# Kernel tuning notes

Hardware: AMD Instinct MI355X
Metric: run time of the kernel (lower is better)

The kernel has to match this reference:

```python
import jax, jax.numpy as jnp
import numpy as np

N_NODES = 50000


def gcn_conv(x, edge_index, W, b):
    # PyG GCNConv: add self-loops, symmetric normalization, linear (no bias), scatter-add, + bias
    n = x.shape[0]
    loops = jnp.arange(n, dtype=edge_index.dtype)
    src = jnp.concatenate([edge_index[0], loops])
    dst = jnp.concatenate([edge_index[1], loops])
    deg = jax.ops.segment_sum(jnp.ones_like(dst, dtype=x.dtype), dst, num_segments=n)
    dinv = jnp.where(deg > 0, jax.lax.rsqrt(deg), 0.0)
    norm = dinv[src] * dinv[dst]                       # [E+N]
    h = x @ W                                          # [N, out]
    msg = h[src] * norm[:, None]                       # [E+N, out]
    return jax.ops.segment_sum(msg, dst, num_segments=n) + b


def setup_inputs() -> dict:
    key = jax.random.key(0)
    k1, k2, k3, k4, k5, k6 = jax.random.split(key, 6)
    z = jax.random.normal(k1, (N_NODES, 64), dtype=jnp.float32)
    edge_index = jax.random.randint(k2, (2, 1600000), 0, N_NODES, dtype=jnp.int64)
    # glorot-ish init for weights
    W1 = jax.random.normal(k3, (64, 128), dtype=jnp.float32) * (1.0 / np.sqrt(64))
    b1 = jnp.zeros((128,), dtype=jnp.float32)
    W2 = jax.random.normal(k4, (128, 64), dtype=jnp.float32) * (1.0 / np.sqrt(128))
    b2 = jnp.zeros((64,), dtype=jnp.float32)
    return {"z": z, "edge_index": edge_index, "W1": W1, "b1": b1, "W2": W2, "b2": b2}


def reference(z, edge_index, W1, b1, W2, b2):
    h = jax.nn.relu(gcn_conv(z, edge_index, W1, b1))
    x_hat = jax.nn.relu(gcn_conv(h, edge_index, W2, b2))
    return x_hat
```

## Files before the change

kernel.cpp:

```cpp
#include <hip/hip_runtime.h>
#include <hip/hip_fp16.h>


#define NBUK 196
#define NPAD (NBUK * 256)
#define BCAP 16384
#define SCAP 32
#define SSH 4
#define SCAP2 32
#define SENT 0xFFFFFFFFu
#define P1GRID 768

struct half4_t { __half2 lo, hi; };
struct half8_t { __half2 h0, h1, h2, h3; };

__global__ void zero_kernel(int* __restrict__ p, int n) {
    int i = blockIdx.x * blockDim.x + threadIdx.x;
    if (i < n) p[i] = 0;
}

__global__ __launch_bounds__(256) void pass1_kernel(
    const int* __restrict__ src, const int* __restrict__ dst,
    unsigned* __restrict__ bucketed, int* __restrict__ gcur,
    unsigned* __restrict__ ovf, int* __restrict__ novf, int E) {
    __shared__ unsigned stage[NBUK * SCAP];
    __shared__ int lcnt[NBUK];
    __shared__ int bbase[NBUK];
    __shared__ unsigned units[512];
    __shared__ int nunits;
    int tid = threadIdx.x;
    for (int i = tid; i < NBUK; i += 256) lcnt[i] = 0;
    if (tid == 0) nunits = 0;
    int per = (E + gridDim.x - 1) / gridDim.x;
    int lo = blockIdx.x * per, hi = min(E, lo + per);
    __syncthreads();
    for (int t0 = lo; t0 < hi; t0 += 2048) {
#pragma unroll
        for (int rep = 0; rep < 8; ++rep) {
            int i = t0 + rep * 256 + tid;
            if (i < hi) {
                int s = src[i], d = dst[i];
                int b = d >> 8;
                unsigned pk = (unsigned)(s & 0xFFFF) | ((unsigned)(d & 0xFF) << 16);
                int pos = atomicAdd(&lcnt[b], 1);
                if (pos < SCAP) {
                    stage[b * SCAP + pos] = pk;
                } else {
                    int op = atomicAdd(novf, 1);
                    if (op < 4096) ovf[op] = pk | ((unsigned)b << 24);
                    atomicSub(&lcnt[b], 1);
                }
            }
        }
        __syncthreads();
        if (tid < NBUK) {
            int c = min(lcnt[tid], SCAP);
            int f = c >> 4;
            if (f > 0) {
                bbase[tid] = atomicAdd(&gcur[tid], f * 16);
                int u0 = atomicAdd(&nunits, f);
                for (int g = 0; g < f; ++g) units[u0 + g] = ((unsigned)tid << 8) | g;
            }
        }
        __syncthreads();
        int nu = nunits;
        for (int u = tid >> 4; u < nu; u += 16) {
            unsigned ds = units[u];
            int b = ds >> 8, g = ds & 0xFF;
            int li = tid & 15;
            int idx = bbase[b] + g * 16 + li;
            if (idx < BCAP)
                bucketed[(size_t)b * BCAP + idx] = stage[b * SCAP + g * 16 + li];
        }
        __syncthreads();
        if (tid < NBUK) {
            int c = min(lcnt[tid], SCAP);
            int f = (c >> 4) << 4;
            int rem = c - f;
            for (int j = 0; j < rem; ++j) stage[tid * SCAP + j] = stage[tid * SCAP + f + j];
            lcnt[tid] = rem;
        }
        if (tid == 0) nunits = 0;
        __syncthreads();
    }
    if (tid < NBUK) {
        int c = min(lcnt[tid], SCAP);
        if (c > 0) {
            for (int j = c; j < 16; ++j) stage[tid * SCAP + j] = SENT;
            bbase[tid] = atomicAdd(&gcur[tid], 16);
            int u0 = atomicAdd(&nunits, 1);
            units[u0] = ((unsigned)tid << 8);
        }
    }
    __syncthreads();
    int nu = nunits;
    for (int u = tid >> 4; u < nu; u += 16) {
        unsigned ds = units[u];
        int b = ds >> 8, g = ds & 0xFF;
        int li = tid & 15;
        int idx = bbase[b] + g * 16 + li;
        if (idx < BCAP)
            bucketed[(size_t)b * BCAP + idx] = stage[b * SCAP + g * 16 + li];
    }
}

__global__ __launch_bounds__(256) void pass2_kernel(
    const unsigned* __restrict__ bucketed, const int* __restrict__ gcur,
    const unsigned* __restrict__ ovf, const int* __restrict__ novf,
    unsigned short* __restrict__ ellg, int* __restrict__ cnt4, int N) {
    __shared__ unsigned short ell[256 * SCAP2];
    __shared__ int lcnt[256];
    int b = blockIdx.x >> 2, q = blockIdx.x & 3;
    int tid = threadIdx.x;
    lcnt[tid] = 0;
    __syncthreads();
    int c = min(gcur[b], BCAP);
    int lo = (c * q) >> 2, hi = (c * (q + 1)) >> 2;
    const unsigned* bp = bucketed + (size_t)b * BCAP;
    for (int j = lo + tid; j < hi; j += 256) {
        unsigned e = bp[j];
        if (e == SENT) continue;
        int r = (e >> 16) & 0xFF;
        int p = atomicAdd(&lcnt[r], 1);
        if (p < SCAP2) ell[r * SCAP2 + p] = (unsigned short)(e & 0xFFFF);
    }
    if (q == 0) {
        int no = min(*novf, 4096);
        for (int j = tid; j < no; j += 256) {
            unsigned e = ovf[j];
            if ((int)(e >> 24) == b) {
                int r = (e >> 16) & 0xFF;
                int p = atomicAdd(&lcnt[r], 1);
                if (p < SCAP2) ell[r * SCAP2 + p] = (unsigned short)(e & 0xFFFF);
            }
        }
    }
    __syncthreads();
    int node = b * 256 + tid;
    if (node < N) cnt4[q * NPAD + node] = lcnt[tid];
    unsigned* eg = (unsigned*)(ellg + ((size_t)q * NPAD + b * 256) * SCAP2);
    const unsigned* el = (const unsigned*)ell;
    for (int k = tid; k < 256 * (SCAP2 / 2); k += 256) eg[k] = el[k];
}

__global__ void dinvps_kernel(const int* __restrict__ cnt4, const float* __restrict__ z,
                              float* __restrict__ dinv, half4_t* __restrict__ zp, int N) {
    int i = blockIdx.x * blockDim.x + threadIdx.x;
    if (i >= N * 16) return;
    int node = i >> 4;
    int deg = cnt4[node] + cnt4[NPAD + node] + cnt4[2 * NPAD + node] + cnt4[3 * NPAD + node];
    float w = rsqrtf((float)(deg + 1));
    if ((i & 15) == 0) dinv[node] = w;
    float4 v = reinterpret_cast<const float4*>(z)[i];
    half4_t h;
    h.lo = __floats2half2_rn(v.x * w, v.y * w);
    h.hi = __floats2half2_rn(v.z * w, v.w * w);
    zp[i] = h;
}

template <int EPI>
__global__ __launch_bounds__(256) void gatherv_kernel(
    const half8_t* __restrict__ rows, const int* __restrict__ cnt4,
    const unsigned short* __restrict__ ell, const float* __restrict__ dinv,
    const float* __restrict__ bias, void* __restrict__ outp, int N) {
    int node = (blockIdx.x * 256 + threadIdx.x) >> 6;
    int lane = threadIdx.x & 63;
    if (node >= N) return;
    int sg = lane >> 3, li = lane & 7;
    int stripe = sg >> 1, par = sg & 1;
    half8_t self = rows[node * 8 + li];
    float a0 = 0.f, a1 = 0.f, a2 = 0.f, a3 = 0.f, a4 = 0.f, a5 = 0.f, a6 = 0.f, a7 = 0.f;
    int cl = min(cnt4[stripe * NPAD + node], SCAP2);
    size_t base = ((size_t)stripe * NPAD + node) * SCAP2;
    int k = par;
    for (; k + 6 < cl; k += 8) {
        int s0 = ell[base + k];
        int s1 = ell[base + k + 2];
        int s2 = ell[base + k + 4];
        int s3 = ell[base + k + 6];
        half8_t v0 = rows[s0 * 8 + li];
        half8_t v1 = rows[s1 * 8 + li];
        half8_t v2 = rows[s2 * 8 + li];
        half8_t v3 = rows[s3 * 8 + li];
        float2 f;
        f = __half22float2(v0.h0); a0 += f.x; a1 += f.y;
        f = __half22float2(v0.h1); a2 += f.x; a3 += f.y;
        f = __half22float2(v0.h2); a4 += f.x; a5 += f.y;
        f = __half22float2(v0.h3); a6 += f.x; a7 += f.y;
        f = __half22float2(v1.h0); a0 += f.x; a1 += f.y;
        f = __half22float2(v1.h1); a2 += f.x; a3 += f.y;
        f = __half22float2(v1.h2); a4 += f.x; a5 += f.y;
        f = __half22float2(v1.h3); a6 += f.x; a7 += f.y;
        f = __half22float2(v2.h0); a0 += f.x; a1 += f.y;
        f = __half22float2(v2.h1); a2 += f.x; a3 += f.y;
        f = __half22float2(v2.h2); a4 += f.x; a5 += f.y;
        f = __half22float2(v2.h3); a6 += f.x; a7 += f.y;
        f = __half22float2(v3.h0); a0 += f.x; a1 += f.y;
        f = __half22float2(v3.h1); a2 += f.x; a3 += f.y;
        f = __half22float2(v3.h2); a4 += f.x; a5 += f.y;
        f = __half22float2(v3.h3); a6 += f.x; a7 += f.y;
    }
    if (k + 2 < cl) {
        int s0 = ell[base + k];
        int s1 = ell[base + k + 2];
        half8_t v0 = rows[s0 * 8 + li];
        half8_t v1 = rows[s1 * 8 + li];
        float2 f;
        f = __half22float2(v0.h0); a0 += f.x; a1 += f.y;
        f = __half22float2(v0.h1); a2 += f.x; a3 += f.y;
        f = __half22float2(v0.h2); a4 += f.x; a5 += f.y;
        f = __half22float2(v0.h3); a6 += f.x; a7 += f.y;
        f = __half22float2(v1.h0); a0 += f.x; a1 += f.y;
        f = __half22float2(v1.h1); a2 += f.x; a3 += f.y;
        f = __half22float2(v1.h2); a4 += f.x; a5 += f.y;
        f = __half22float2(v1.h3); a6 += f.x; a7 += f.y;
        k += 4;
    }
    if (k < cl) {
        int s = ell[base + k];
        half8_t v = rows[s * 8 + li];
        float2 f;
        f = __half22float2(v.h0); a0 += f.x; a1 += f.y;
        f = __half22float2(v.h1); a2 += f.x; a3 += f.y;
        f = __half22float2(v.h2); a4 += f.x; a5 += f.y;
        f = __half22float2(v.h3); a6 += f.x; a7 += f.y;
    }
#pragma unroll
    for (int off = 8; off < 64; off <<= 1) {
        a0 += __shfl_xor(a0, off, 64);
        a1 += __shfl_xor(a1, off, 64);
        a2 += __shfl_xor(a2, off, 64);
        a3 += __shfl_xor(a3, off, 64);
        a4 += __shfl_xor(a4, off, 64);
        a5 += __shfl_xor(a5, off, 64);
        a6 += __shfl_xor(a6, off, 64);
        a7 += __shfl_xor(a7, off, 64);
    }
    float w = dinv[node];
    {
        float2 f;
        f = __half22float2(self.h0); a0 += f.x; a1 += f.y;
        f = __half22float2(self.h1); a2 += f.x; a3 += f.y;
        f = __half22float2(self.h2); a4 += f.x; a5 += f.y;
        f = __half22float2(self.h3); a6 += f.x; a7 += f.y;
    }
    if (sg != 0) return;
    if constexpr (EPI == 1) {
        float4 b0 = reinterpret_cast<const float4*>(bias)[li * 2];
        float4 b1 = reinterpret_cast<const float4*>(bias)[li * 2 + 1];
        float4 o0, o1;
        o0.x = fmaxf(fmaf(a0, w, b0.x), 0.f);
        o0.y = fmaxf(fmaf(a1, w, b0.y), 0.f);
        o0.z = fmaxf(fmaf(a2, w, b0.z), 0.f);
        o0.w = fmaxf(fmaf(a3, w, b0.w), 0.f);
        o1.x = fmaxf(fmaf(a4, w, b1.x), 0.f);
        o1.y = fmaxf(fmaf(a5, w, b1.y), 0.f);
        o1.z = fmaxf(fmaf(a6, w, b1.z), 0.f);
        o1.w = fmaxf(fmaf(a7, w, b1.w), 0.f);
        reinterpret_cast<float4*>(outp)[node * 16 + li * 2] = o0;
        reinterpret_cast<float4*>(outp)[node * 16 + li * 2 + 1] = o1;
    } else {
        half8_t h;
        h.h0 = __floats2half2_rn(a0 * w, a1 * w);
        h.h1 = __floats2half2_rn(a2 * w, a3 * w);
        h.h2 = __floats2half2_rn(a4 * w, a5 * w);
        h.h3 = __floats2half2_rn(a6 * w, a7 * w);
        reinterpret_cast<half8_t*>(outp)[node * 8 + li] = h;
    }
}

__global__ __launch_bounds__(256) void gemm1_kernel(
    const half4_t* __restrict__ agg1, const float* __restrict__ W,
    const float* __restrict__ b1, __half* __restrict__ x1, int N) {
    __shared__ float wl[64 * 128];
    __shared__ float zl[16 * 64];
    __shared__ float bl[128];
    int tid = threadIdx.x;
    for (int i = tid; i < 64 * 128; i += 256) wl[i] = W[i];
    if (tid < 128) bl[tid] = b1[tid];
    int base = blockIdx.x * 16;
    {
        int r = tid >> 4, c4 = tid & 15;
        int node = base + r;
        float4 f4 = make_float4(0.f, 0.f, 0.f, 0.f);
        if (node < N) {
            half4_t h = agg1[node * 16 + c4];
            float2 lo = __half22float2(h.lo), hi = __half22float2(h.hi);
            f4 = make_float4(lo.x, lo.y, hi.x, hi.y);
        }
        float* zr = &zl[r * 64 + c4 * 4];
        zr[0] = f4.x; zr[1] = f4.y; zr[2] = f4.z; zr[3] = f4.w;
    }
    __syncthreads();
    int j = tid & 127, rb = tid >> 7;
    float acc[8];
#pragma unroll
    for (int k = 0; k < 8; ++k) acc[k] = 0.f;
    for (int kk = 0; kk < 64; ++kk) {
        float wv = wl[kk * 128 + j];
#pragma unroll
        for (int k = 0; k < 8; ++k)
            acc[k] = fmaf(zl[(rb + 2 * k) * 64 + kk], wv, acc[k]);
    }
#pragma unroll
    for (int k = 0; k < 8; ++k) {
        int node = base + rb + 2 * k;
        if (node < N) x1[node * 128 + j] = __float2half_rn(fmaxf(acc[k] + bl[j], 0.f));
    }
}

__global__ __launch_bounds__(256) void gemm2_kernel(
    const __half* __restrict__ x1, const float* __restrict__ dinv,
    const float* __restrict__ W, __half* __restrict__ h2, int N) {
    __shared__ float wl[128 * 64];
    __shared__ float xl[16 * 128];
    int tid = threadIdx.x;
    for (int i = tid; i < 128 * 64; i += 256) wl[i] = W[i];
    int base = blockIdx.x * 16;
    const half4_t* x4 = reinterpret_cast<const half4_t*>(x1);
    for (int idx = tid; idx < 512; idx += 256) {
        int r = idx >> 5, c4 = idx & 31;
        int node = base + r;
        float4 f4 = make_float4(0.f, 0.f, 0.f, 0.f);
        if (node < N) {
            half4_t h = x4[node * 32 + c4];
            float2 lo = __half22float2(h.lo), hi = __half22float2(h.hi);
            f4 = make_float4(lo.x, lo.y, hi.x, hi.y);
        }
        float* xr = &xl[r * 128 + c4 * 4];
        xr[0] = f4.x; xr[1] = f4.y; xr[2] = f4.z; xr[3] = f4.w;
    }
    __syncthreads();
    int j = tid & 63, rb = tid >> 6;
    float acc[4] = {0.f, 0.f, 0.f, 0.f};
    for (int kk = 0; kk < 128; ++kk) {
        float wv = wl[kk * 64 + j];
#pragma unroll
        for (int k = 0; k < 4; ++k)
            acc[k] = fmaf(xl[(rb + 4 * k) * 128 + kk], wv, acc[k]);
    }
#pragma unroll
    for (int k = 0; k < 4; ++k) {
        int node = base + rb + 4 * k;
        if (node < N) h2[node * 64 + j] = __float2half_rn(acc[k] * dinv[node]);
    }
}

extern "C" void kernel_launch(void* const* d_in, const int* in_sizes, int n_in,
                              void* d_out, int out_size, void* d_ws, size_t ws_size,
                              hipStream_t stream) {
    const float* z  = (const float*)d_in[0];
    const int* edges = (const int*)d_in[1];
    const float* W1 = (const float*)d_in[2];
    const float* b1 = (const float*)d_in[3];
    const float* W2 = (const float*)d_in[4];
    const float* b2 = (const float*)d_in[5];
    float* out = (float*)d_out;

    int N = in_sizes[0] / 64;
    int E = in_sizes[1] / 2;
    const int* src = edges;
    const int* dst = edges + E;

    const size_t MB = 1024 * 1024;
    char* ws = (char*)d_ws;
    int*            gcur = (int*)(ws);
    int*            novf = (int*)(ws + 4 * 1024);
    unsigned*       ovf  = (unsigned*)(ws + 8 * 1024);
    int*            cnt4 = (int*)(ws + 1 * MB);
    float*          dinv = (float*)(ws + 2 * MB);
    unsigned short* ellg = (unsigned short*)(ws + 3 * MB);
    half4_t*        zp   = (half4_t*)(ws + 16 * MB);
    half4_t*        agg1 = (half4_t*)(ws + 23 * MB);
    __half*         x1   = (__half*)(ws + 30 * MB);
    unsigned*       bucketed = (unsigned*)(ws + 43 * MB);
    __half*         h2   = (__half*)agg1;

    zero_kernel<<<5, 256, 0, stream>>>(gcur, 1025);
    pass1_kernel<<<P1GRID, 256, 0, stream>>>(src, dst, bucketed, gcur, ovf, novf, E);
    pass2_kernel<<<NBUK * SSH, 256, 0, stream>>>(bucketed, gcur, ovf, novf, ellg, cnt4, N);
    dinvps_kernel<<<(N * 16 + 255) / 256, 256, 0, stream>>>(cnt4, z, dinv, zp, N);

    gatherv_kernel<0><<<(N + 3) / 4, 256, 0, stream>>>((const half8_t*)zp, cnt4, ellg, dinv, nullptr, agg1, N);
    gemm1_kernel<<<(N + 15) / 16, 256, 0, stream>>>(agg1, W1, b1, x1, N);
    gemm2_kernel<<<(N + 15) / 16, 256, 0, stream>>>(x1, dinv, W2, h2, N);
    gatherv_kernel<1><<<(N + 3) / 4, 256, 0, stream>>>((const half8_t*)h2, cnt4, ellg, dinv, b2, out, N);
}
```

Measured before the change: 168.3 us.

## Use MFMA fp16 matrix cores for both dense GEMMs with pre-transposed half weights

Replaces the scalar-FMA shared-memory GEMMs with MFMA 16x16x32 fp16 instructions, tiling 64 nodes per block across four wavefronts. A new prep kernel zeroes the counters and writes transposed fp16 copies of W1 and W2 once per call, so each block loads half-precision weights with padded LDS rows instead of re-reading fp32 weights. The aim is to cut per-block weight loading and ALU work in the GEMM stages. Weights are now rounded to fp16, which adds some precision loss.

```diff
diff --git a/kernel.cpp b/kernel.cpp
--- a/kernel.cpp
+++ b/kernel.cpp
@@ -14,9 +14,23 @@
 struct half4_t { __half2 lo, hi; };
 struct half8_t { __half2 h0, h1, h2, h3; };
 
-__global__ void zero_kernel(int* __restrict__ p, int n) {
-    int i = blockIdx.x * blockDim.x + threadIdx.x;
-    if (i < n) p[i] = 0;
+typedef _Float16 f16x8 __attribute__((ext_vector_type(8)));
+typedef float f32x4 __attribute__((ext_vector_type(4)));
+union FragU { f16x8 v; uint2 q[2]; };
+
+__global__ void prep_kernel(const float* __restrict__ W1, const float* __restrict__ W2,
+                            _Float16* __restrict__ W1T, _Float16* __restrict__ W2T,
+                            int* __restrict__ gcur) {
+    int i = blockIdx.x * 256 + threadIdx.x;
+    if (i < 1025) gcur[i] = 0;
+    if (i < 8192) {
+        int n = i >> 6, k = i & 63;
+        W1T[n * 64 + k] = (_Float16)W1[k * 128 + n];
+    } else if (i < 16384) {
+        int j = i - 8192;
+        int n = j >> 7, k = j & 127;
+        W2T[n * 128 + k] = (_Float16)W2[k * 64 + n];
+    }
 }
 
 __global__ __launch_bounds__(256) void pass1_kernel(
@@ -270,79 +284,112 @@
 }
 
 __global__ __launch_bounds__(256) void gemm1_kernel(
-    const half4_t* __restrict__ agg1, const float* __restrict__ W,
+    const half8_t* __restrict__ agg1, const _Float16* __restrict__ W1T,
     const float* __restrict__ b1, __half* __restrict__ x1, int N) {
-    __shared__ float wl[64 * 128];
-    __shared__ float zl[16 * 64];
+    __shared__ _Float16 al[64 * 72];
+    __shared__ _Float16 wt[128 * 72];
     __shared__ float bl[128];
     int tid = threadIdx.x;
-    for (int i = tid; i < 64 * 128; i += 256) wl[i] = W[i];
+    int base = blockIdx.x * 64;
+    for (int i = tid; i < 64 * 8; i += 256) {
+        int r = i >> 3, c8 = i & 7;
+        int node = base + r;
+        half8_t h = {};
+        if (node < N) h = agg1[node * 8 + c8];
+        *reinterpret_cast<half8_t*>(&al[r * 72 + c8 * 8]) = h;
+    }
+    for (int i = tid; i < 128 * 8; i += 256) {
+        int n = i >> 3, c8 = i & 7;
+        *reinterpret_cast<half8_t*>(&wt[n * 72 + c8 * 8]) =
+            reinterpret_cast<const half8_t*>(W1T)[n * 8 + c8];
+    }
     if (tid < 128) bl[tid] = b1[tid];
-    int base = blockIdx.x * 16;
-    {
-        int r = tid >> 4, c4 = tid & 15;
+    __syncthreads();
+    int w = tid >> 6, l = tid & 63;
+    int row = w * 16 + (l & 15);
+    int kq = (l >> 4) * 4;
+    f32x4 acc[8];
+#pragma unroll
+    for (int ct = 0; ct < 8; ++ct) acc[ct] = (f32x4){0.f, 0.f, 0.f, 0.f};
+#pragma unroll
+    for (int kh = 0; kh < 2; ++kh) {
+        FragU a;
+        a.q[0] = *reinterpret_cast<const uint2*>(&al[row * 72 + kh * 32 + kq]);
+        a.q[1] = *reinterpret_cast<const uint2*>(&al[row * 72 + kh * 32 + 16 + kq]);
+#pragma unroll
+        for (int ct = 0; ct < 8; ++ct) {
+            int col = ct * 16 + (l & 15);
+            FragU b;
+            b.q[0] = *reinterpret_cast<const uint2*>(&wt[col * 72 + kh * 32 + kq]);
+            b.q[1] = *reinterpret_cast<const uint2*>(&wt[col * 72 + kh * 32 + 16 + kq]);
+            acc[ct] = __builtin_amdgcn_mfma_f32_16x16x32_f16(a.v, b.v, acc[ct], 0, 0, 0);
+        }
+    }
+    int orow = w * 16 + (l >> 4) * 4;
+#pragma unroll
+    for (int ct = 0; ct < 8; ++ct) {
+        int col = ct * 16 + (l & 15);
+#pragma unroll
+        for (int j = 0; j < 4; ++j) {
+            int node = base + orow + j;
+            if (node < N)
+                x1[node * 128 + col] = __float2half_rn(fmaxf(acc[ct][j] + bl[col], 0.f));
+        }
+    }
+}
+
+__global__ __launch_bounds__(256) void gemm2_kernel(
+    const half8_t* __restrict__ x1, const float* __restrict__ dinv,
+    const _Float16* __restrict__ W2T, __half* __restrict__ h2, int N) {
+    __shared__ _Float16 al[64 * 136];
+    __shared__ _Float16 wt[64 * 136];
+    __shared__ float dl[64];
+    int tid = threadIdx.x;
+    int base = blockIdx.x * 64;
+    for (int i = tid; i < 64 * 16; i += 256) {
+        int r = i >> 4, c8 = i & 15;
         int node = base + r;
-        float4 f4 = make_float4(0.f, 0.f, 0.f, 0.f);
-        if (node < N) {
-            half4_t h = agg1[node * 16 + c4];
-            float2 lo = __half22float2(h.lo), hi = __half22float2(h.hi);
-            f4 = make_float4(lo.x, lo.y, hi.x, hi.y);
-        }
-        float* zr = &zl[r * 64 + c4 * 4];
-        zr[0] = f4.x; zr[1] = f4.y; zr[2] = f4.z; zr[3] = f4.w;
-    }
-    __syncthreads();
-    int j = tid & 127, rb = tid >> 7;
-    float acc[8];
-#pragma unroll
-    for (int k = 0; k < 8; ++k) acc[k] = 0.f;
-    for (int kk = 0; kk < 64; ++kk) {
-        float wv = wl[kk * 128 + j];
-#pragma unroll
-        for (int k = 0; k < 8; ++k)
-            acc[k] = fmaf(zl[(rb + 2 * k) * 64 + kk], wv, acc[k]);
-    }
-#pragma unroll
-    for (int k = 0; k < 8; ++k) {
-        int node = base + rb + 2 * k;
-        if (node < N) x1[node * 128 + j] = __float2half_rn(fmaxf(acc[k] + bl[j], 0.f));
-    }
-}
-
-__global__ __launch_bounds__(256) void gemm2_kernel(
-    const __half* __restrict__ x1, const float* __restrict__ dinv,
-    const float* __restrict__ W, __half* __restrict__ h2, int N) {
-    __shared__ float wl[128 * 64];
-    __shared__ float xl[16 * 128];
-    int tid = threadIdx.x;
-    for (int i = tid; i < 128 * 64; i += 256) wl[i] = W[i];
-    int base = blockIdx.x * 16;
-    const half4_t* x4 = reinterpret_cast<const half4_t*>(x1);
-    for (int idx = tid; idx < 512; idx += 256) {
-        int r = idx >> 5, c4 = idx & 31;
-        int node = base + r;
-        float4 f4 = make_float4(0.f, 0.f, 0.f, 0.f);
-        if (node < N) {
-            half4_t h = x4[node * 32 + c4];
-            float2 lo = __half22float2(h.lo), hi = __half22float2(h.hi);
-            f4 = make_float4(lo.x, lo.y, hi.x, hi.y);
-        }
-        float* xr = &xl[r * 128 + c4 * 4];
-        xr[0] = f4.x; xr[1] = f4.y; xr[2] = f4.z; xr[3] = f4.w;
-    }
-    __syncthreads();
-    int j = tid & 63, rb = tid >> 6;
-    float acc[4] = {0.f, 0.f, 0.f, 0.f};
-    for (int kk = 0; kk < 128; ++kk) {
-        float wv = wl[kk * 64 + j];
-#pragma unroll
-        for (int k = 0; k < 4; ++k)
-            acc[k] = fmaf(xl[(rb + 4 * k) * 128 + kk], wv, acc[k]);
-    }
-#pragma unroll
-    for (int k = 0; k < 4; ++k) {
-        int node = base + rb + 4 * k;
-        if (node < N) h2[node * 64 + j] = __float2half_rn(acc[k] * dinv[node]);
+        half8_t h = {};
+        if (node < N) h = x1[node * 16 + c8];
+        *reinterpret_cast<half8_t*>(&al[r * 136 + c8 * 8]) = h;
+    }
+    for (int i = tid; i < 64 * 16; i += 256) {
+        int n = i >> 4, c8 = i & 15;
+        *reinterpret_cast<half8_t*>(&wt[n * 136 + c8 * 8]) =
+            reinterpret_cast<const half8_t*>(W2T)[n * 16 + c8];
+    }
+    if (tid < 64) dl[tid] = (base + tid < N) ? dinv[base + tid] : 0.f;
+    __syncthreads();
+    int w = tid >> 6, l = tid & 63;
+    int row = w * 16 + (l & 15);
+    int kq = (l >> 4) * 4;
+    f32x4 acc[4];
+#pragma unroll
+    for (int ct = 0; ct < 4; ++ct) acc[ct] = (f32x4){0.f, 0.f, 0.f, 0.f};
+#pragma unroll
+    for (int kh = 0; kh < 4; ++kh) {
+        FragU a;
+        a.q[0] = *reinterpret_cast<const uint2*>(&al[row * 136 + kh * 32 + kq]);
+        a.q[1] = *reinterpret_cast<const uint2*>(&al[row * 136 + kh * 32 + 16 + kq]);
+#pragma unroll
+        for (int ct = 0; ct < 4; ++ct) {
+            int col = ct * 16 + (l & 15);
+            FragU b;
+            b.q[0] = *reinterpret_cast<const uint2*>(&wt[col * 136 + kh * 32 + kq]);
+            b.q[1] = *reinterpret_cast<const uint2*>(&wt[col * 136 + kh * 32 + 16 + kq]);
+            acc[ct] = __builtin_amdgcn_mfma_f32_16x16x32_f16(a.v, b.v, acc[ct], 0, 0, 0);
+        }
+    }
+    int orow = w * 16 + (l >> 4) * 4;
+#pragma unroll
+    for (int ct = 0; ct < 4; ++ct) {
+        int col = ct * 16 + (l & 15);
+#pragma unroll
+        for (int j = 0; j < 4; ++j) {
+            int node = base + orow + j;
+            if (node < N)
+                h2[node * 64 + col] = __float2half_rn(acc[ct][j] * dl[orow + j]);
+        }
     }
 }
 
@@ -374,15 +421,17 @@
     half4_t*        agg1 = (half4_t*)(ws + 23 * MB);
     __half*         x1   = (__half*)(ws + 30 * MB);
     unsigned*       bucketed = (unsigned*)(ws + 43 * MB);
+    _Float16*       W1T  = (_Float16*)(ws + 56 * MB);
+    _Float16*       W2T  = (_Float16*)(ws + 56 * MB + 32 * 1024);
     __half*         h2   = (__half*)agg1;
 
-    zero_kernel<<<5, 256, 0, stream>>>(gcur, 1025);
+    prep_kernel<<<64, 256, 0, stream>>>(W1, W2, W1T, W2T, gcur);
     pass1_kernel<<<P1GRID, 256, 0, stream>>>(src, dst, bucketed, gcur, ovf, novf, E);
     pass2_kernel<<<NBUK * SSH, 256, 0, stream>>>(bucketed, gcur, ovf, novf, ellg, cnt4, N);
     dinvps_kernel<<<(N * 16 + 255) / 256, 256, 0, stream>>>(cnt4, z, dinv, zp, N);
 
     gatherv_kernel<0><<<(N + 3) / 4, 256, 0, stream>>>((const half8_t*)zp, cnt4, ellg, dinv, nullptr, agg1, N);
-    gemm1_kernel<<<(N + 15) / 16, 256, 0, stream>>>(agg1, W1, b1, x1, N);
-    gemm2_kernel<<<(N + 15) / 16, 256, 0, stream>>>(x1, dinv, W2, h2, N);
+    gemm1_kernel<<<(N + 63) / 64, 256, 0, stream>>>((const half8_t*)agg1, W1T, b1, x1, N);
+    gemm2_kernel<<<(N + 63) / 64, 256, 0, stream>>>((const half8_t*)x1, dinv, W2T, h2, N);
     gatherv_kernel<1><<<(N + 3) / 4, 256, 0, stream>>>((const half8_t*)h2, cnt4, ellg, dinv, b2, out, N);
 }
```

Result: slower. 185.6 us (+10.3%).
